# Kernel tuning notes

Measured on AMD Instinct MI355X. Metric: run time of the kernel, lower is better.

Reference implementation:

```python
import jax, jax.numpy as jnp
import numpy as np

B, L, H, NH = 2, 256, 1024, 16
HD = H // NH


def _ln(x, g, b, eps=1e-5):
    m = x.mean(-1, keepdims=True)
    v = x.var(-1, keepdims=True)
    return (x - m) * jax.lax.rsqrt(v + eps) * g + b


def setup_inputs() -> dict:
    key = jax.random.key(0)
    ks = jax.random.split(key, 24)
    s = 0.02
    inp = {
        'x': jax.random.normal(ks[0], (B, L, H), jnp.float32),
        'mask': jnp.ones((B, 1, 1, L), dtype=bool),
        'pos_emb': jax.random.normal(ks[1], (B, L, L, H), jnp.float32),
        'Wq': jax.random.normal(ks[2], (H, H), jnp.float32) * s,
        'bq': jnp.zeros((H,), jnp.float32),
        'Wk': jax.random.normal(ks[3], (H, H), jnp.float32) * s,
        'bk': jnp.zeros((H,), jnp.float32),
        'Wv': jax.random.normal(ks[4], (H, H), jnp.float32) * s,
        'bv': jnp.zeros((H,), jnp.float32),
        'Wr': jax.random.normal(ks[5], (H, H), jnp.float32) * s,
        'br': jnp.zeros((H,), jnp.float32),
        'u': jax.random.normal(ks[6], (NH, HD), jnp.float32) * s,
        'vb': jax.random.normal(ks[7], (NH, HD), jnp.float32) * s,
        'Wo': jax.random.normal(ks[8], (H, H), jnp.float32) * s,
        'bo': jnp.zeros((H,), jnp.float32),
        'ln1_g': jnp.ones((H,), jnp.float32),
        'ln1_b': jnp.zeros((H,), jnp.float32),
        'W1': jax.random.normal(ks[9], (3 * H, H), jnp.float32) * s,
        'b1': jnp.zeros((3 * H,), jnp.float32),
        'W2': jax.random.normal(ks[10], (H, 3 * H), jnp.float32) * s,
        'b2': jnp.zeros((H,), jnp.float32),
        'ln2_g': jnp.ones((H,), jnp.float32),
        'ln2_b': jnp.zeros((H,), jnp.float32),
    }
    return inp


def reference(x, mask, pos_emb, Wq, bq, Wk, bk, Wv, bv, Wr, br, u, vb, Wo, bo,
              ln1_g, ln1_b, W1, b1, W2, b2, ln2_g, ln2_b):
    b, l, h = x.shape
    nh, hd = NH, h // NH

    def heads(t):  # [B,L,H] -> [B,nh,L,hd]
        return t.reshape(b, l, nh, hd).transpose(0, 2, 1, 3)

    q = heads(x @ Wq.T + bq)
    k = heads(x @ Wk.T + bk)
    v = heads(x @ Wv.T + bv)
    # relative keys: [B,Lq,Lk,H] -> [B,Lq,Lk,nh,hd]
    rk = (pos_emb @ Wr.T + br).reshape(b, l, l, nh, hd)

    u4 = u[None, :, None, :]   # [1,nh,1,hd]
    v4 = vb[None, :, None, :]
    content = jnp.einsum('bhqd,bhkd->bhqk', q + u4, k)
    position = jnp.einsum('bhqd,bqkhd->bhqk', q + v4, rk)
    attn = jnp.where(mask, content + position, -1e6)
    attn = jax.nn.softmax(attn, axis=-1)  # attn_drop inactive (eval)

    out = jnp.einsum('bhqk,bhkd->bhqd', attn, v)
    out = out.transpose(0, 2, 1, 3).reshape(b, l, h)
    out = jax.nn.leaky_relu(out @ Wo.T + bo, 0.01) + x
    out = _ln(out, ln1_g, ln1_b)
    x2 = out
    out = jax.nn.leaky_relu(out @ W1.T + b1, 0.01) @ W2.T + b2
    out = _ln(out + x2, ln2_g, ln2_b)
    return out
```

## Files before the change

### kernel.cpp

```cpp
#include <hip/hip_runtime.h>
#include <cstdint>
#include <cstddef>

#define B_  2
#define L_  256
#define H_  1024
#define NH_ 16
#define HD_ 64
#define M_  (B_ * L_)

__device__ __forceinline__
void gemm64_body(const float* __restrict__ A, const float* __restrict__ Bw,
                 const float* __restrict__ bias, const float* __restrict__ resid,
                 float* __restrict__ C, int N, int K, int act,
                 int row0, int col0, float As[16][68], float Bs[16][68])
{
    const int tid = threadIdx.x;
    const int tx = tid & 15, ty = tid >> 4;
    const int lr = tid >> 2;
    const int lc = (tid & 3) * 4;
    float acc[4][4] = {};
    for (int k0 = 0; k0 < K; k0 += 16) {
        float4 av = *(const float4*)(A  + (size_t)(row0 + lr) * K + k0 + lc);
        float4 bv = *(const float4*)(Bw + (size_t)(col0 + lr) * K + k0 + lc);
        As[lc+0][lr] = av.x; As[lc+1][lr] = av.y; As[lc+2][lr] = av.z; As[lc+3][lr] = av.w;
        Bs[lc+0][lr] = bv.x; Bs[lc+1][lr] = bv.y; Bs[lc+2][lr] = bv.z; Bs[lc+3][lr] = bv.w;
        __syncthreads();
        #pragma unroll
        for (int kk = 0; kk < 16; ++kk) {
            float4 a4 = *(const float4*)&As[kk][ty * 4];
            float4 b4 = *(const float4*)&Bs[kk][tx * 4];
            float a[4] = {a4.x, a4.y, a4.z, a4.w};
            float b[4] = {b4.x, b4.y, b4.z, b4.w};
            #pragma unroll
            for (int i = 0; i < 4; ++i)
                #pragma unroll
                for (int j = 0; j < 4; ++j)
                    acc[i][j] = fmaf(a[i], b[j], acc[i][j]);
        }
        __syncthreads();
    }
    #pragma unroll
    for (int j = 0; j < 4; ++j) {
        const int c = col0 + tx * 4 + j;
        const float bj = bias ? bias[c] : 0.0f;
        #pragma unroll
        for (int i = 0; i < 4; ++i) {
            const int r = row0 + ty * 4 + i;
            float v = acc[i][j] + bj;
            if (act) v = v > 0.0f ? v : 0.01f * v;
            if (resid) v += resid[(size_t)r * N + c];
            C[(size_t)r * N + c] = v;
        }
    }
}

__global__ __launch_bounds__(256)
void gemm_bt(const float* __restrict__ A, const float* __restrict__ Bw,
             const float* __restrict__ bias, const float* __restrict__ resid,
             float* __restrict__ C, int M, int N, int K, int act)
{
    __shared__ float As[16][68];
    __shared__ float Bs[16][68];
    gemm64_body(A, Bw, bias, resid, C, N, K, act,
                blockIdx.y * 64, blockIdx.x * 64, As, Bs);
}

__global__ __launch_bounds__(256)
void qkv_kernel(const float* __restrict__ x,
                const float* __restrict__ Wq, const float* __restrict__ bq,
                const float* __restrict__ Wk, const float* __restrict__ bk,
                const float* __restrict__ Wv, const float* __restrict__ bv,
                float* __restrict__ qb, float* __restrict__ kb, float* __restrict__ vbuf)
{
    __shared__ float As[16][68];
    __shared__ float Bs[16][68];
    const int z = blockIdx.z;
    const float* Bw   = (z == 0) ? Wq : (z == 1) ? Wk : Wv;
    const float* bias = (z == 0) ? bq : (z == 1) ? bk : bv;
    float*       C    = (z == 0) ? qb : (z == 1) ? kb : vbuf;
    gemm64_body(x, Bw, bias, nullptr, C, H_, H_, 0,
                blockIdx.y * 64, blockIdx.x * 64, As, Bs);
}

__global__ __launch_bounds__(256)
void s_kernel(const float* __restrict__ qbuf, const float* __restrict__ vb,
              const float* __restrict__ Wr, float* __restrict__ sbuf)
{
    __shared__ float As[64][68];
    __shared__ float Bs[64][68];
    const int tid = threadIdx.x;
    const int h  = blockIdx.z;
    const int e0 = blockIdx.x * 64;
    const int m0 = blockIdx.y * 64;
    #pragma unroll
    for (int p = 0; p < 4; ++p) {
        int f4 = tid + p * 256;
        int r  = f4 >> 4;
        int c  = (f4 & 15) * 4;
        float4 qv  = *(const float4*)(qbuf + (size_t)(m0 + r) * H_ + h * HD_ + c);
        float4 vbv = *(const float4*)(vb + h * HD_ + c);
        As[c+0][r] = qv.x + vbv.x; As[c+1][r] = qv.y + vbv.y;
        As[c+2][r] = qv.z + vbv.z; As[c+3][r] = qv.w + vbv.w;
        float4 wv = *(const float4*)(Wr + (size_t)(h * HD_ + r) * H_ + e0 + c);
        *(float4*)&Bs[r][c] = wv;
    }
    __syncthreads();
    const int tx = tid & 15, ty = tid >> 4;
    float acc[4][4] = {};
    #pragma unroll 16
    for (int kk = 0; kk < 64; ++kk) {
        float4 a4 = *(const float4*)&As[kk][ty * 4];
        float4 b4 = *(const float4*)&Bs[kk][tx * 4];
        float a[4] = {a4.x, a4.y, a4.z, a4.w};
        float b[4] = {b4.x, b4.y, b4.z, b4.w};
        #pragma unroll
        for (int i = 0; i < 4; ++i)
            #pragma unroll
            for (int j = 0; j < 4; ++j)
                acc[i][j] = fmaf(a[i], b[j], acc[i][j]);
    }
    #pragma unroll
    for (int i = 0; i < 4; ++i)
        #pragma unroll
        for (int j = 0; j < 4; ++j)
            sbuf[((size_t)(m0 + ty*4 + i) * NH_ + h) * H_ + e0 + tx*4 + j] = acc[i][j];
}

__global__ __launch_bounds__(256)
void cpos_kernel(const float* __restrict__ qbuf, const float* __restrict__ vb,
                 const float* __restrict__ br, float* __restrict__ cpos)
{
    const int idx = blockIdx.x * 256 + threadIdx.x;
    const int m = idx >> 4, h = idx & 15;
    float s = 0.0f;
    #pragma unroll 8
    for (int d = 0; d < HD_; ++d)
        s += (qbuf[(size_t)m * H_ + h * HD_ + d] + vb[h * HD_ + d]) * br[h * HD_ + d];
    cpos[idx] = s;
}

__global__ __launch_bounds__(256)
void content_kernel(const float* __restrict__ qbuf, const float* __restrict__ kbuf,
                    const float* __restrict__ u, const float* __restrict__ cpos,
                    float* __restrict__ scores)
{
    __shared__ float As[64][68];
    __shared__ float Bs[64][68];
    const int tid = threadIdx.x;
    const int bh = blockIdx.z; const int b = bh >> 4, h = bh & 15;
    const int q0 = blockIdx.y * 64, k0 = blockIdx.x * 64;
    #pragma unroll
    for (int p = 0; p < 4; ++p) {
        int f4 = tid + p * 256;
        int r  = f4 >> 4;
        int c  = (f4 & 15) * 4;
        float4 qv = *(const float4*)(qbuf + (size_t)(b * L_ + q0 + r) * H_ + h * HD_ + c);
        float4 uv = *(const float4*)(u + h * HD_ + c);
        As[c+0][r] = qv.x + uv.x; As[c+1][r] = qv.y + uv.y;
        As[c+2][r] = qv.z + uv.z; As[c+3][r] = qv.w + uv.w;
        float4 kv = *(const float4*)(kbuf + (size_t)(b * L_ + k0 + r) * H_ + h * HD_ + c);
        Bs[c+0][r] = kv.x; Bs[c+1][r] = kv.y; Bs[c+2][r] = kv.z; Bs[c+3][r] = kv.w;
    }
    __syncthreads();
    const int tx = tid & 15, ty = tid >> 4;
    float acc[4][4] = {};
    #pragma unroll 16
    for (int kk = 0; kk < 64; ++kk) {
        float4 a4 = *(const float4*)&As[kk][ty * 4];
        float4 b4 = *(const float4*)&Bs[kk][tx * 4];
        float a[4] = {a4.x, a4.y, a4.z, a4.w};
        float b[4] = {b4.x, b4.y, b4.z, b4.w};
        #pragma unroll
        for (int i = 0; i < 4; ++i)
            #pragma unroll
            for (int j = 0; j < 4; ++j)
                acc[i][j] = fmaf(a[i], b[j], acc[i][j]);
    }
    #pragma unroll
    for (int i = 0; i < 4; ++i) {
        const int qrow = q0 + ty * 4 + i;
        const float cp = cpos[(size_t)(b * L_ + qrow) * NH_ + h];
        #pragma unroll
        for (int j = 0; j < 4; ++j)
            scores[(((size_t)b * NH_ + h) * L_ + qrow) * L_ + k0 + tx*4 + j] = acc[i][j] + cp;
    }
}

__global__ __launch_bounds__(256)
void pos_kernel(const float* __restrict__ sbuf, const float* __restrict__ pos_emb,
                float* __restrict__ scores)
{
    __shared__ float sP[128][33];
    __shared__ float sS[16][33];
    const int m = blockIdx.x;
    const int b = m >> 8, q = m & 255;
    const int kb0 = blockIdx.y * 128;
    const int tid = threadIdx.x;
    const int hg = tid >> 6;
    const int kg = tid & 63;
    float acc[4][2] = {};
    for (int e0 = 0; e0 < H_; e0 += 32) {
        {
            int hh = tid >> 4;
            int e2 = (tid & 15) * 2;
            float2 sv = *(const float2*)(sbuf + ((size_t)m * NH_ + hh) * H_ + e0 + e2);
            sS[hh][e2] = sv.x; sS[hh][e2 + 1] = sv.y;
        }
        #pragma unroll
        for (int p = 0; p < 4; ++p) {
            int idx = p * 256 + tid;
            int row = idx >> 3;
            int e4  = (idx & 7) * 4;
            float4 pv = *(const float4*)(pos_emb + ((size_t)m * L_ + kb0 + row) * H_ + e0 + e4);
            sP[row][e4+0] = pv.x; sP[row][e4+1] = pv.y; sP[row][e4+2] = pv.z; sP[row][e4+3] = pv.w;
        }
        __syncthreads();
        #pragma unroll
        for (int e = 0; e < 32; ++e) {
            float sv[4], pv[2];
            #pragma unroll
            for (int j = 0; j < 4; ++j) sv[j] = sS[hg * 4 + j][e];
            #pragma unroll
            for (int i = 0; i < 2; ++i) pv[i] = sP[kg + i * 64][e];
            #pragma unroll
            for (int j = 0; j < 4; ++j)
                #pragma unroll
                for (int i = 0; i < 2; ++i)
                    acc[j][i] = fmaf(sv[j], pv[i], acc[j][i]);
        }
        __syncthreads();
    }
    #pragma unroll
    for (int j = 0; j < 4; ++j) {
        const int h = hg * 4 + j;
        #pragma unroll
        for (int i = 0; i < 2; ++i) {
            const int k = kb0 + kg + i * 64;
            scores[(((size_t)b * NH_ + h) * L_ + q) * L_ + k] += acc[j][i];
        }
    }
}

__global__ __launch_bounds__(64)
void softmax_kernel(float* __restrict__ scores)
{
    const size_t row = blockIdx.x;
    const int t = threadIdx.x;
    float4 v = *(float4*)(scores + row * L_ + t * 4);
    float mx = fmaxf(fmaxf(v.x, v.y), fmaxf(v.z, v.w));
    #pragma unroll
    for (int off = 32; off >= 1; off >>= 1) mx = fmaxf(mx, __shfl_xor(mx, off));
    v.x = __expf(v.x - mx); v.y = __expf(v.y - mx);
    v.z = __expf(v.z - mx); v.w = __expf(v.w - mx);
    float s = v.x + v.y + v.z + v.w;
    #pragma unroll
    for (int off = 32; off >= 1; off >>= 1) s += __shfl_xor(s, off);
    const float inv = 1.0f / s;
    v.x *= inv; v.y *= inv; v.z *= inv; v.w *= inv;
    *(float4*)(scores + row * L_ + t * 4) = v;
}

__global__ __launch_bounds__(256)
void attnv_kernel(const float* __restrict__ scores, const float* __restrict__ vbuf,
                  float* __restrict__ attno)
{
    __shared__ float As[64][68];
    __shared__ float Bs[64][68];
    const int bh = blockIdx.y; const int b = bh >> 4, h = bh & 15;
    const int q0 = blockIdx.x * 64;
    const int tid = threadIdx.x;
    const int tx = tid & 15, ty = tid >> 4;
    float acc[4][4] = {};
    for (int k0 = 0; k0 < L_; k0 += 64) {
        #pragma unroll
        for (int p = 0; p < 4; ++p) {
            int f4 = tid + p * 256;
            int r  = f4 >> 4;
            int c  = (f4 & 15) * 4;
            float4 pv = *(const float4*)(scores + (((size_t)b * NH_ + h) * L_ + q0 + r) * L_ + k0 + c);
            As[c+0][r] = pv.x; As[c+1][r] = pv.y; As[c+2][r] = pv.z; As[c+3][r] = pv.w;
            float4 vv = *(const float4*)(vbuf + (size_t)(b * L_ + k0 + r) * H_ + h * HD_ + c);
            *(float4*)&Bs[r][c] = vv;
        }
        __syncthreads();
        #pragma unroll 16
        for (int kk = 0; kk < 64; ++kk) {
            float4 a4 = *(const float4*)&As[kk][ty * 4];
            float4 b4 = *(const float4*)&Bs[kk][tx * 4];
            float a[4] = {a4.x, a4.y, a4.z, a4.w};
            float bb[4] = {b4.x, b4.y, b4.z, b4.w};
            #pragma unroll
            for (int i = 0; i < 4; ++i)
                #pragma unroll
                for (int j = 0; j < 4; ++j)
                    acc[i][j] = fmaf(a[i], bb[j], acc[i][j]);
        }
        __syncthreads();
    }
    #pragma unroll
    for (int i = 0; i < 4; ++i)
        #pragma unroll
        for (int j = 0; j < 4; ++j)
            attno[(size_t)(b * L_ + q0 + ty*4 + i) * H_ + h * HD_ + tx*4 + j] = acc[i][j];
}

__global__ __launch_bounds__(256)
void ln_kernel(const float* __restrict__ in, const float* __restrict__ resid,
               const float* __restrict__ g, const float* __restrict__ bias,
               float* __restrict__ out)
{
    __shared__ float rsum[4], rsum2[4];
    const size_t row = blockIdx.x;
    const int tid = threadIdx.x;
    float4 v = *(const float4*)(in + row * H_ + tid * 4);
    if (resid) {
        float4 r = *(const float4*)(resid + row * H_ + tid * 4);
        v.x += r.x; v.y += r.y; v.z += r.z; v.w += r.w;
    }
    float s  = v.x + v.y + v.z + v.w;
    float s2 = v.x*v.x + v.y*v.y + v.z*v.z + v.w*v.w;
    #pragma unroll
    for (int off = 32; off >= 1; off >>= 1) {
        s  += __shfl_xor(s, off);
        s2 += __shfl_xor(s2, off);
    }
    const int w = tid >> 6;
    if ((tid & 63) == 0) { rsum[w] = s; rsum2[w] = s2; }
    __syncthreads();
    s  = rsum[0] + rsum[1] + rsum[2] + rsum[3];
    s2 = rsum2[0] + rsum2[1] + rsum2[2] + rsum2[3];
    const float mean = s * (1.0f / H_);
    const float var  = s2 * (1.0f / H_) - mean * mean;
    const float rs   = rsqrtf(var + 1e-5f);
    float4 gv = *(const float4*)(g + tid * 4);
    float4 bv = *(const float4*)(bias + tid * 4);
    float4 o;
    o.x = (v.x - mean) * rs * gv.x + bv.x;
    o.y = (v.y - mean) * rs * gv.y + bv.y;
    o.z = (v.z - mean) * rs * gv.z + bv.z;
    o.w = (v.w - mean) * rs * gv.w + bv.w;
    *(float4*)(out + row * H_ + tid * 4) = o;
}

extern "C" void kernel_launch(void* const* d_in, const int* in_sizes, int n_in,
                              void* d_out, int out_size, void* d_ws, size_t ws_size,
                              hipStream_t stream)
{
    const float* x       = (const float*)d_in[0];
    const float* pos_emb = (const float*)d_in[2];
    const float* Wq = (const float*)d_in[3];  const float* bq = (const float*)d_in[4];
    const float* Wk = (const float*)d_in[5];  const float* bk = (const float*)d_in[6];
    const float* Wv = (const float*)d_in[7];  const float* bv = (const float*)d_in[8];
    const float* Wr = (const float*)d_in[9];  const float* br = (const float*)d_in[10];
    const float* u  = (const float*)d_in[11]; const float* vb = (const float*)d_in[12];
    const float* Wo = (const float*)d_in[13]; const float* bo = (const float*)d_in[14];
    const float* g1 = (const float*)d_in[15]; const float* be1 = (const float*)d_in[16];
    const float* W1 = (const float*)d_in[17]; const float* b1 = (const float*)d_in[18];
    const float* W2 = (const float*)d_in[19]; const float* b2 = (const float*)d_in[20];
    const float* g2 = (const float*)d_in[21]; const float* be2 = (const float*)d_in[22];
    float* outp = (float*)d_out;

    float* ws     = (float*)d_ws;
    float* qbuf   = ws;
    float* kbuf   = qbuf + (size_t)M_ * H_;
    float* vbuf   = kbuf + (size_t)M_ * H_;
    float* sbuf   = vbuf + (size_t)M_ * H_;
    float* cpos   = sbuf + (size_t)M_ * NH_ * H_;
    float* scores = cpos + (size_t)M_ * NH_;
    float* attno  = scores + (size_t)B_ * NH_ * L_ * L_;
    float* o1     = attno + (size_t)M_ * H_;
    float* x2     = o1 + (size_t)M_ * H_;
    float* hid    = x2 + (size_t)M_ * H_;
    float* o2     = hid + (size_t)M_ * 3 * H_;

    dim3 thr(256);

    qkv_kernel<<<dim3(16, 8, 3), thr, 0, stream>>>(x, Wq, bq, Wk, bk, Wv, bv,
                                                   qbuf, kbuf, vbuf);

    s_kernel<<<dim3(16, 8, 16), thr, 0, stream>>>(qbuf, vb, Wr, sbuf);
    cpos_kernel<<<dim3(32), thr, 0, stream>>>(qbuf, vb, br, cpos);

    content_kernel<<<dim3(4, 4, 32), thr, 0, stream>>>(qbuf, kbuf, u, cpos, scores);
    pos_kernel<<<dim3(M_, 2), thr, 0, stream>>>(sbuf, pos_emb, scores);

    softmax_kernel<<<dim3(B_ * NH_ * L_), dim3(64), 0, stream>>>(scores);
    attnv_kernel<<<dim3(4, 32), thr, 0, stream>>>(scores, vbuf, attno);

    gemm_bt<<<dim3(16, 8), thr, 0, stream>>>(attno, Wo, bo, x, o1, M_, H_, H_, 1);
    ln_kernel<<<dim3(M_), thr, 0, stream>>>(o1, nullptr, g1, be1, x2);

    gemm_bt<<<dim3(48, 8), thr, 0, stream>>>(x2, W1, b1, nullptr, hid, M_, 3 * H_, H_, 1);
    gemm_bt<<<dim3(16, 8), thr, 0, stream>>>(hid, W2, b2, nullptr, o2, M_, H_, 3 * H_, 0);
    ln_kernel<<<dim3(M_), thr, 0, stream>>>(o2, x2, g2, be2, outp);
}
```

Baseline: 1.231 ms.

## Replace LDS-tiled GEMMs with direct-load dot4 kernels, split-K, and restructured pos kernel

The shared-memory tiled GEMMs are replaced by register-only kernels that read float4 strips of A and W straight from global memory, relying on cache for reuse. The Wo and W2 projections use a two-way split-K, and their partial sums are reduced inside fused layernorm kernels that also apply bias, activation and residual. The pos-score kernel now splits the embedding dimension in half, keeps all 16 heads in registers per thread, and writes two partial score planes. The softmax sums those planes, which replaces the read-modify-write on scores. In exchange it uses more workspace and extra partial-buffer traffic, and the direct global loads may cost more than the old LDS tiling.

```diff
diff --git a/kernel.cpp b/kernel.cpp
--- a/kernel.cpp
+++ b/kernel.cpp
@@ -10,77 +10,139 @@
 #define M_  (B_ * L_)
 
 __device__ __forceinline__
-void gemm64_body(const float* __restrict__ A, const float* __restrict__ Bw,
-                 const float* __restrict__ bias, const float* __restrict__ resid,
-                 float* __restrict__ C, int N, int K, int act,
-                 int row0, int col0, float As[16][68], float Bs[16][68])
-{
-    const int tid = threadIdx.x;
-    const int tx = tid & 15, ty = tid >> 4;
-    const int lr = tid >> 2;
-    const int lc = (tid & 3) * 4;
-    float acc[4][4] = {};
-    for (int k0 = 0; k0 < K; k0 += 16) {
-        float4 av = *(const float4*)(A  + (size_t)(row0 + lr) * K + k0 + lc);
-        float4 bv = *(const float4*)(Bw + (size_t)(col0 + lr) * K + k0 + lc);
-        As[lc+0][lr] = av.x; As[lc+1][lr] = av.y; As[lc+2][lr] = av.z; As[lc+3][lr] = av.w;
-        Bs[lc+0][lr] = bv.x; Bs[lc+1][lr] = bv.y; Bs[lc+2][lr] = bv.z; Bs[lc+3][lr] = bv.w;
-        __syncthreads();
-        #pragma unroll
-        for (int kk = 0; kk < 16; ++kk) {
-            float4 a4 = *(const float4*)&As[kk][ty * 4];
-            float4 b4 = *(const float4*)&Bs[kk][tx * 4];
-            float a[4] = {a4.x, a4.y, a4.z, a4.w};
-            float b[4] = {b4.x, b4.y, b4.z, b4.w};
-            #pragma unroll
-            for (int i = 0; i < 4; ++i)
-                #pragma unroll
-                for (int j = 0; j < 4; ++j)
-                    acc[i][j] = fmaf(a[i], b[j], acc[i][j]);
-        }
-        __syncthreads();
-    }
+void dot4_core(const float* __restrict__ A, int lda,
+               const float* __restrict__ Bw, int ldb,
+               int kBeg, int kEnd, int row0, int col0,
+               float acc[4][4])
+{
+    const int tx = threadIdx.x & 15, ty = threadIdx.x >> 4;
+    const float* a0 = A + (size_t)(row0 + ty * 4) * lda;
+    const float* b0 = Bw + (size_t)(col0 + tx * 4) * ldb;
+    #pragma unroll 4
+    for (int k0 = kBeg; k0 < kEnd; k0 += 4) {
+        float4 a[4], b[4];
+        #pragma unroll
+        for (int i = 0; i < 4; ++i) a[i] = *(const float4*)(a0 + (size_t)i * lda + k0);
+        #pragma unroll
+        for (int j = 0; j < 4; ++j) b[j] = *(const float4*)(b0 + (size_t)j * ldb + k0);
+        #pragma unroll
+        for (int i = 0; i < 4; ++i)
+            #pragma unroll
+            for (int j = 0; j < 4; ++j) {
+                acc[i][j] = fmaf(a[i].x, b[j].x, acc[i][j]);
+                acc[i][j] = fmaf(a[i].y, b[j].y, acc[i][j]);
+                acc[i][j] = fmaf(a[i].z, b[j].z, acc[i][j]);
+                acc[i][j] = fmaf(a[i].w, b[j].w, acc[i][j]);
+            }
+    }
+}
+
+__global__ __launch_bounds__(256)
+void qkv_dot4(const float* __restrict__ x,
+              const float* __restrict__ Wq, const float* __restrict__ bq,
+              const float* __restrict__ Wk, const float* __restrict__ bk,
+              const float* __restrict__ Wv, const float* __restrict__ bv,
+              float* __restrict__ qb, float* __restrict__ kb, float* __restrict__ vb)
+{
+    const int z = blockIdx.z;
+    const float* W    = (z == 0) ? Wq : (z == 1) ? Wk : Wv;
+    const float* bias = (z == 0) ? bq : (z == 1) ? bk : bv;
+    float*       C    = (z == 0) ? qb : (z == 1) ? kb : vb;
+    const int row0 = blockIdx.y * 64, col0 = blockIdx.x * 64;
+    float acc[4][4] = {};
+    dot4_core(x, H_, W, H_, 0, H_, row0, col0, acc);
+    const int tx = threadIdx.x & 15, ty = threadIdx.x >> 4;
     #pragma unroll
     for (int j = 0; j < 4; ++j) {
         const int c = col0 + tx * 4 + j;
-        const float bj = bias ? bias[c] : 0.0f;
+        const float bj = bias[c];
+        #pragma unroll
+        for (int i = 0; i < 4; ++i)
+            C[(size_t)(row0 + ty * 4 + i) * H_ + c] = acc[i][j] + bj;
+    }
+}
+
+__global__ __launch_bounds__(256)
+void w1_dot4(const float* __restrict__ x2, const float* __restrict__ W1,
+             const float* __restrict__ b1, float* __restrict__ hid)
+{
+    const int row0 = blockIdx.y * 64, col0 = blockIdx.x * 64;
+    float acc[4][4] = {};
+    dot4_core(x2, H_, W1, H_, 0, H_, row0, col0, acc);
+    const int tx = threadIdx.x & 15, ty = threadIdx.x >> 4;
+    #pragma unroll
+    for (int j = 0; j < 4; ++j) {
+        const int c = col0 + tx * 4 + j;
+        const float bj = b1[c];
         #pragma unroll
         for (int i = 0; i < 4; ++i) {
-            const int r = row0 + ty * 4 + i;
             float v = acc[i][j] + bj;
-            if (act) v = v > 0.0f ? v : 0.01f * v;
-            if (resid) v += resid[(size_t)r * N + c];
-            C[(size_t)r * N + c] = v;
-        }
-    }
-}
-
-__global__ __launch_bounds__(256)
-void gemm_bt(const float* __restrict__ A, const float* __restrict__ Bw,
-             const float* __restrict__ bias, const float* __restrict__ resid,
-             float* __restrict__ C, int M, int N, int K, int act)
-{
-    __shared__ float As[16][68];
-    __shared__ float Bs[16][68];
-    gemm64_body(A, Bw, bias, resid, C, N, K, act,
-                blockIdx.y * 64, blockIdx.x * 64, As, Bs);
-}
-
-__global__ __launch_bounds__(256)
-void qkv_kernel(const float* __restrict__ x,
-                const float* __restrict__ Wq, const float* __restrict__ bq,
-                const float* __restrict__ Wk, const float* __restrict__ bk,
-                const float* __restrict__ Wv, const float* __restrict__ bv,
-                float* __restrict__ qb, float* __restrict__ kb, float* __restrict__ vbuf)
-{
-    __shared__ float As[16][68];
-    __shared__ float Bs[16][68];
+            v = v > 0.0f ? v : 0.01f * v;
+            hid[(size_t)(row0 + ty * 4 + i) * (3 * H_) + c] = v;
+        }
+    }
+}
+
+__global__ __launch_bounds__(256)
+void gemm_dot4_splitk(const float* __restrict__ A, int K,
+                      const float* __restrict__ W, int N,
+                      float* __restrict__ pbase)
+{
     const int z = blockIdx.z;
-    const float* Bw   = (z == 0) ? Wq : (z == 1) ? Wk : Wv;
-    const float* bias = (z == 0) ? bq : (z == 1) ? bk : bv;
-    float*       C    = (z == 0) ? qb : (z == 1) ? kb : vbuf;
-    gemm64_body(x, Bw, bias, nullptr, C, H_, H_, 0,
-                blockIdx.y * 64, blockIdx.x * 64, As, Bs);
+    const int kh = K >> 1;
+    const int row0 = blockIdx.y * 64, col0 = blockIdx.x * 64;
+    float acc[4][4] = {};
+    dot4_core(A, K, W, K, z * kh, z * kh + kh, row0, col0, acc);
+    float* C = pbase + (size_t)z * M_ * N;
+    const int tx = threadIdx.x & 15, ty = threadIdx.x >> 4;
+    #pragma unroll
+    for (int j = 0; j < 4; ++j)
+        #pragma unroll
+        for (int i = 0; i < 4; ++i)
+            C[(size_t)(row0 + ty * 4 + i) * N + col0 + tx * 4 + j] = acc[i][j];
+}
+
+__global__ __launch_bounds__(256)
+void content_dot4(const float* __restrict__ qbuf, const float* __restrict__ kbuf,
+                  const float* __restrict__ u, const float* __restrict__ cpos,
+                  float* __restrict__ scores)
+{
+    const int bh = blockIdx.z; const int b = bh >> 4, h = bh & 15;
+    const int q0 = blockIdx.y * 64, k0 = blockIdx.x * 64;
+    const int tx = threadIdx.x & 15, ty = threadIdx.x >> 4;
+    const float* A  = qbuf + (size_t)(b * L_ + q0 + ty * 4) * H_ + h * HD_;
+    const float* Bp = kbuf + (size_t)(b * L_ + k0 + tx * 4) * H_ + h * HD_;
+    const float* up = u + h * HD_;
+    float acc[4][4] = {};
+    #pragma unroll 4
+    for (int d0 = 0; d0 < HD_; d0 += 4) {
+        float4 uu = *(const float4*)(up + d0);
+        float4 a[4], bb[4];
+        #pragma unroll
+        for (int i = 0; i < 4; ++i) {
+            a[i] = *(const float4*)(A + (size_t)i * H_ + d0);
+            a[i].x += uu.x; a[i].y += uu.y; a[i].z += uu.z; a[i].w += uu.w;
+        }
+        #pragma unroll
+        for (int j = 0; j < 4; ++j) bb[j] = *(const float4*)(Bp + (size_t)j * H_ + d0);
+        #pragma unroll
+        for (int i = 0; i < 4; ++i)
+            #pragma unroll
+            for (int j = 0; j < 4; ++j) {
+                acc[i][j] = fmaf(a[i].x, bb[j].x, acc[i][j]);
+                acc[i][j] = fmaf(a[i].y, bb[j].y, acc[i][j]);
+                acc[i][j] = fmaf(a[i].z, bb[j].z, acc[i][j]);
+                acc[i][j] = fmaf(a[i].w, bb[j].w, acc[i][j]);
+            }
+    }
+    #pragma unroll
+    for (int i = 0; i < 4; ++i) {
+        const int qrow = q0 + ty * 4 + i;
+        const float cp = cpos[(size_t)(b * L_ + qrow) * NH_ + h];
+        #pragma unroll
+        for (int j = 0; j < 4; ++j)
+            scores[(((size_t)b * NH_ + h) * L_ + qrow) * L_ + k0 + tx * 4 + j] = acc[i][j] + cp;
+    }
 }
 
 __global__ __launch_bounds__(256)
@@ -141,124 +203,117 @@
 }
 
 __global__ __launch_bounds__(256)
-void content_kernel(const float* __restrict__ qbuf, const float* __restrict__ kbuf,
-                    const float* __restrict__ u, const float* __restrict__ cpos,
-                    float* __restrict__ scores)
-{
-    __shared__ float As[64][68];
-    __shared__ float Bs[64][68];
+void pos_v2(const float* __restrict__ sbuf, const float* __restrict__ pos_emb,
+            float* __restrict__ pp)
+{
+    __shared__ float sP[256][33];
+    __shared__ float sS[32][16];
+    const int m = blockIdx.x;  const int b = m >> 8, q = m & 255;
+    const int eh = blockIdx.y;
     const int tid = threadIdx.x;
-    const int bh = blockIdx.z; const int b = bh >> 4, h = bh & 15;
-    const int q0 = blockIdx.y * 64, k0 = blockIdx.x * 64;
-    #pragma unroll
-    for (int p = 0; p < 4; ++p) {
-        int f4 = tid + p * 256;
-        int r  = f4 >> 4;
-        int c  = (f4 & 15) * 4;
-        float4 qv = *(const float4*)(qbuf + (size_t)(b * L_ + q0 + r) * H_ + h * HD_ + c);
-        float4 uv = *(const float4*)(u + h * HD_ + c);
-        As[c+0][r] = qv.x + uv.x; As[c+1][r] = qv.y + uv.y;
-        As[c+2][r] = qv.z + uv.z; As[c+3][r] = qv.w + uv.w;
-        float4 kv = *(const float4*)(kbuf + (size_t)(b * L_ + k0 + r) * H_ + h * HD_ + c);
-        Bs[c+0][r] = kv.x; Bs[c+1][r] = kv.y; Bs[c+2][r] = kv.z; Bs[c+3][r] = kv.w;
+    const int w = tid >> 6, lane = tid & 63;
+    const float* Pm = pos_emb + (size_t)m * L_ * H_;
+    const float* Sm = sbuf + (size_t)m * NH_ * H_;
+    float acc[16][4] = {};
+    for (int c = 0; c < 16; ++c) {
+        const int e0 = eh * 512 + c * 32;
+        if (tid < 128) {
+            int hh = tid >> 3;
+            int e4 = (tid & 7) * 4;
+            float4 sv = *(const float4*)(Sm + (size_t)hh * H_ + e0 + e4);
+            sS[e4+0][hh] = sv.x; sS[e4+1][hh] = sv.y;
+            sS[e4+2][hh] = sv.z; sS[e4+3][hh] = sv.w;
+        }
+        #pragma unroll
+        for (int p = 0; p < 8; ++p) {
+            int idx = p * 256 + tid;
+            int kk = idx >> 3;
+            int ec = (idx & 7) * 4;
+            float4 pv = *(const float4*)(Pm + (size_t)kk * H_ + e0 + ec);
+            sP[kk][ec+0] = pv.x; sP[kk][ec+1] = pv.y;
+            sP[kk][ec+2] = pv.z; sP[kk][ec+3] = pv.w;
+        }
+        __syncthreads();
+        #pragma unroll
+        for (int ee = 0; ee < 8; ++ee) {
+            const int el = w * 8 + ee;
+            float s[16];
+            #pragma unroll
+            for (int j4 = 0; j4 < 4; ++j4) {
+                float4 s4 = *(const float4*)&sS[el][j4 * 4];
+                s[j4*4+0] = s4.x; s[j4*4+1] = s4.y; s[j4*4+2] = s4.z; s[j4*4+3] = s4.w;
+            }
+            #pragma unroll
+            for (int i = 0; i < 4; ++i) {
+                const float pk = sP[lane + i * 64][el];
+                #pragma unroll
+                for (int h = 0; h < 16; ++h)
+                    acc[h][i] = fmaf(s[h], pk, acc[h][i]);
+            }
+        }
+        __syncthreads();
+    }
+    float* red = &sP[0][0];
+    if (w >= 2) {
+        float* dst = red + (size_t)(w - 2) * 4096;
+        #pragma unroll
+        for (int h = 0; h < 16; ++h)
+            #pragma unroll
+            for (int i = 0; i < 4; ++i)
+                dst[(h * 4 + i) * 64 + lane] = acc[h][i];
     }
     __syncthreads();
-    const int tx = tid & 15, ty = tid >> 4;
-    float acc[4][4] = {};
-    #pragma unroll 16
-    for (int kk = 0; kk < 64; ++kk) {
-        float4 a4 = *(const float4*)&As[kk][ty * 4];
-        float4 b4 = *(const float4*)&Bs[kk][tx * 4];
-        float a[4] = {a4.x, a4.y, a4.z, a4.w};
-        float b[4] = {b4.x, b4.y, b4.z, b4.w};
-        #pragma unroll
-        for (int i = 0; i < 4; ++i)
-            #pragma unroll
-            for (int j = 0; j < 4; ++j)
-                acc[i][j] = fmaf(a[i], b[j], acc[i][j]);
-    }
-    #pragma unroll
-    for (int i = 0; i < 4; ++i) {
-        const int qrow = q0 + ty * 4 + i;
-        const float cp = cpos[(size_t)(b * L_ + qrow) * NH_ + h];
-        #pragma unroll
-        for (int j = 0; j < 4; ++j)
-            scores[(((size_t)b * NH_ + h) * L_ + qrow) * L_ + k0 + tx*4 + j] = acc[i][j] + cp;
-    }
-}
-
-__global__ __launch_bounds__(256)
-void pos_kernel(const float* __restrict__ sbuf, const float* __restrict__ pos_emb,
-                float* __restrict__ scores)
-{
-    __shared__ float sP[128][33];
-    __shared__ float sS[16][33];
-    const int m = blockIdx.x;
-    const int b = m >> 8, q = m & 255;
-    const int kb0 = blockIdx.y * 128;
-    const int tid = threadIdx.x;
-    const int hg = tid >> 6;
-    const int kg = tid & 63;
-    float acc[4][2] = {};
-    for (int e0 = 0; e0 < H_; e0 += 32) {
-        {
-            int hh = tid >> 4;
-            int e2 = (tid & 15) * 2;
-            float2 sv = *(const float2*)(sbuf + ((size_t)m * NH_ + hh) * H_ + e0 + e2);
-            sS[hh][e2] = sv.x; sS[hh][e2 + 1] = sv.y;
-        }
-        #pragma unroll
-        for (int p = 0; p < 4; ++p) {
-            int idx = p * 256 + tid;
-            int row = idx >> 3;
-            int e4  = (idx & 7) * 4;
-            float4 pv = *(const float4*)(pos_emb + ((size_t)m * L_ + kb0 + row) * H_ + e0 + e4);
-            sP[row][e4+0] = pv.x; sP[row][e4+1] = pv.y; sP[row][e4+2] = pv.z; sP[row][e4+3] = pv.w;
-        }
-        __syncthreads();
-        #pragma unroll
-        for (int e = 0; e < 32; ++e) {
-            float sv[4], pv[2];
-            #pragma unroll
-            for (int j = 0; j < 4; ++j) sv[j] = sS[hg * 4 + j][e];
-            #pragma unroll
-            for (int i = 0; i < 2; ++i) pv[i] = sP[kg + i * 64][e];
-            #pragma unroll
-            for (int j = 0; j < 4; ++j)
-                #pragma unroll
-                for (int i = 0; i < 2; ++i)
-                    acc[j][i] = fmaf(sv[j], pv[i], acc[j][i]);
-        }
-        __syncthreads();
-    }
-    #pragma unroll
-    for (int j = 0; j < 4; ++j) {
-        const int h = hg * 4 + j;
-        #pragma unroll
-        for (int i = 0; i < 2; ++i) {
-            const int k = kb0 + kg + i * 64;
-            scores[(((size_t)b * NH_ + h) * L_ + q) * L_ + k] += acc[j][i];
-        }
+    if (w < 2) {
+        const float* src = red + (size_t)w * 4096;
+        #pragma unroll
+        for (int h = 0; h < 16; ++h)
+            #pragma unroll
+            for (int i = 0; i < 4; ++i)
+                acc[h][i] += src[(h * 4 + i) * 64 + lane];
+    }
+    __syncthreads();
+    if (w == 1) {
+        #pragma unroll
+        for (int h = 0; h < 16; ++h)
+            #pragma unroll
+            for (int i = 0; i < 4; ++i)
+                red[(h * 4 + i) * 64 + lane] = acc[h][i];
+    }
+    __syncthreads();
+    if (w == 0) {
+        float* ppe = pp + (size_t)eh * B_ * NH_ * L_ * L_;
+        #pragma unroll
+        for (int h = 0; h < 16; ++h)
+            #pragma unroll
+            for (int i = 0; i < 4; ++i) {
+                float vsum = acc[h][i] + red[(h * 4 + i) * 64 + lane];
+                ppe[(((size_t)(b * NH_ + h)) * L_ + q) * L_ + lane + i * 64] = vsum;
+            }
     }
 }
 
 __global__ __launch_bounds__(64)
-void softmax_kernel(float* __restrict__ scores)
+void softmax3(float* __restrict__ scores, const float* __restrict__ pp0,
+              const float* __restrict__ pp1)
 {
     const size_t row = blockIdx.x;
     const int t = threadIdx.x;
-    float4 v = *(float4*)(scores + row * L_ + t * 4);
+    const size_t off = row * L_ + t * 4;
+    float4 v = *(float4*)(scores + off);
+    float4 a = *(const float4*)(pp0 + off);
+    float4 b = *(const float4*)(pp1 + off);
+    v.x += a.x + b.x; v.y += a.y + b.y; v.z += a.z + b.z; v.w += a.w + b.w;
     float mx = fmaxf(fmaxf(v.x, v.y), fmaxf(v.z, v.w));
     #pragma unroll
-    for (int off = 32; off >= 1; off >>= 1) mx = fmaxf(mx, __shfl_xor(mx, off));
+    for (int off2 = 32; off2 >= 1; off2 >>= 1) mx = fmaxf(mx, __shfl_xor(mx, off2));
     v.x = __expf(v.x - mx); v.y = __expf(v.y - mx);
     v.z = __expf(v.z - mx); v.w = __expf(v.w - mx);
     float s = v.x + v.y + v.z + v.w;
     #pragma unroll
-    for (int off = 32; off >= 1; off >>= 1) s += __shfl_xor(s, off);
+    for (int off2 = 32; off2 >= 1; off2 >>= 1) s += __shfl_xor(s, off2);
     const float inv = 1.0f / s;
     v.x *= inv; v.y *= inv; v.z *= inv; v.w *= inv;
-    *(float4*)(scores + row * L_ + t * 4) = v;
+    *(float4*)(scores + off) = v;
 }
 
 __global__ __launch_bounds__(256)
@@ -305,19 +360,11 @@
             attno[(size_t)(b * L_ + q0 + ty*4 + i) * H_ + h * HD_ + tx*4 + j] = acc[i][j];
 }
 
-__global__ __launch_bounds__(256)
-void ln_kernel(const float* __restrict__ in, const float* __restrict__ resid,
-               const float* __restrict__ g, const float* __restrict__ bias,
-               float* __restrict__ out)
+__device__ __forceinline__
+void ln_core(float4 v, const float* __restrict__ g, const float* __restrict__ bias,
+             float* __restrict__ out, size_t row, int tid)
 {
     __shared__ float rsum[4], rsum2[4];
-    const size_t row = blockIdx.x;
-    const int tid = threadIdx.x;
-    float4 v = *(const float4*)(in + row * H_ + tid * 4);
-    if (resid) {
-        float4 r = *(const float4*)(resid + row * H_ + tid * 4);
-        v.x += r.x; v.y += r.y; v.z += r.z; v.w += r.w;
-    }
     float s  = v.x + v.y + v.z + v.w;
     float s2 = v.x*v.x + v.y*v.y + v.z*v.z + v.w*v.w;
     #pragma unroll
@@ -343,6 +390,48 @@
     *(float4*)(out + row * H_ + tid * 4) = o;
 }
 
+__global__ __launch_bounds__(256)
+void ln1_fuse(const float* __restrict__ p0, const float* __restrict__ p1,
+              const float* __restrict__ bo, const float* __restrict__ x,
+              const float* __restrict__ g, const float* __restrict__ bias,
+              float* __restrict__ out)
+{
+    const size_t row = blockIdx.x;
+    const int tid = threadIdx.x;
+    const size_t off = row * H_ + tid * 4;
+    float4 a = *(const float4*)(p0 + off);
+    float4 b = *(const float4*)(p1 + off);
+    float4 bb = *(const float4*)(bo + tid * 4);
+    float4 xx = *(const float4*)(x + off);
+    float4 v;
+    v.x = a.x + b.x + bb.x; v.y = a.y + b.y + bb.y;
+    v.z = a.z + b.z + bb.z; v.w = a.w + b.w + bb.w;
+    v.x = (v.x > 0.f ? v.x : 0.01f * v.x) + xx.x;
+    v.y = (v.y > 0.f ? v.y : 0.01f * v.y) + xx.y;
+    v.z = (v.z > 0.f ? v.z : 0.01f * v.z) + xx.z;
+    v.w = (v.w > 0.f ? v.w : 0.01f * v.w) + xx.w;
+    ln_core(v, g, bias, out, row, tid);
+}
+
+__global__ __launch_bounds__(256)
+void ln2_fuse(const float* __restrict__ p0, const float* __restrict__ p1,
+              const float* __restrict__ b2, const float* __restrict__ x2,
+              const float* __restrict__ g, const float* __restrict__ bias,
+              float* __restrict__ out)
+{
+    const size_t row = blockIdx.x;
+    const int tid = threadIdx.x;
+    const size_t off = row * H_ + tid * 4;
+    float4 a = *(const float4*)(p0 + off);
+    float4 b = *(const float4*)(p1 + off);
+    float4 bb = *(const float4*)(b2 + tid * 4);
+    float4 xx = *(const float4*)(x2 + off);
+    float4 v;
+    v.x = a.x + b.x + bb.x + xx.x; v.y = a.y + b.y + bb.y + xx.y;
+    v.z = a.z + b.z + bb.z + xx.z; v.w = a.w + b.w + bb.w + xx.w;
+    ln_core(v, g, bias, out, row, tid);
+}
+
 extern "C" void kernel_launch(void* const* d_in, const int* in_sizes, int n_in,
                               void* d_out, int out_size, void* d_ws, size_t ws_size,
                               hipStream_t stream)
@@ -363,35 +452,36 @@
 
     float* ws     = (float*)d_ws;
     float* qbuf   = ws;
-    float* kbuf   = qbuf + (size_t)M_ * H_;
-    float* vbuf   = kbuf + (size_t)M_ * H_;
-    float* sbuf   = vbuf + (size_t)M_ * H_;
-    float* cpos   = sbuf + (size_t)M_ * NH_ * H_;
-    float* scores = cpos + (size_t)M_ * NH_;
-    float* attno  = scores + (size_t)B_ * NH_ * L_ * L_;
-    float* o1     = attno + (size_t)M_ * H_;
-    float* x2     = o1 + (size_t)M_ * H_;
-    float* hid    = x2 + (size_t)M_ * H_;
-    float* o2     = hid + (size_t)M_ * 3 * H_;
+    float* kbuf   = qbuf  + (size_t)M_ * H_;
+    float* vbuf   = kbuf  + (size_t)M_ * H_;
+    float* sbuf   = vbuf  + (size_t)M_ * H_;
+    float* cpos   = sbuf  + (size_t)M_ * NH_ * H_;
+    float* scores = cpos  + (size_t)M_ * NH_;
+    float* pp     = scores + (size_t)B_ * NH_ * L_ * L_;
+    float* attno  = pp    + (size_t)2 * B_ * NH_ * L_ * L_;
+    float* o1p    = attno + (size_t)M_ * H_;
+    float* x2     = o1p   + (size_t)2 * M_ * H_;
+    float* hid    = x2    + (size_t)M_ * H_;
+    float* o2p    = hid   + (size_t)M_ * 3 * H_;
 
     dim3 thr(256);
 
-    qkv_kernel<<<dim3(16, 8, 3), thr, 0, stream>>>(x, Wq, bq, Wk, bk, Wv, bv,
-                                                   qbuf, kbuf, vbuf);
-
+    qkv_dot4<<<dim3(16, 8, 3), thr, 0, stream>>>(x, Wq, bq, Wk, bk, Wv, bv,
+                                                 qbuf, kbuf, vbuf);
     s_kernel<<<dim3(16, 8, 16), thr, 0, stream>>>(qbuf, vb, Wr, sbuf);
     cpos_kernel<<<dim3(32), thr, 0, stream>>>(qbuf, vb, br, cpos);
 
-    content_kernel<<<dim3(4, 4, 32), thr, 0, stream>>>(qbuf, kbuf, u, cpos, scores);
-    pos_kernel<<<dim3(M_, 2), thr, 0, stream>>>(sbuf, pos_emb, scores);
-
-    softmax_kernel<<<dim3(B_ * NH_ * L_), dim3(64), 0, stream>>>(scores);
+    content_dot4<<<dim3(4, 4, 32), thr, 0, stream>>>(qbuf, kbuf, u, cpos, scores);
+    pos_v2<<<dim3(M_, 2), thr, 0, stream>>>(sbuf, pos_emb, pp);
+
+    softmax3<<<dim3(B_ * NH_ * L_), dim3(64), 0, stream>>>(
+        scores, pp, pp + (size_t)B_ * NH_ * L_ * L_);
     attnv_kernel<<<dim3(4, 32), thr, 0, stream>>>(scores, vbuf, attno);
 
-    gemm_bt<<<dim3(16, 8), thr, 0, stream>>>(attno, Wo, bo, x, o1, M_, H_, H_, 1);
-    ln_kernel<<<dim3(M_), thr, 0, stream>>>(o1, nullptr, g1, be1, x2);
-
-    gemm_bt<<<dim3(48, 8), thr, 0, stream>>>(x2, W1, b1, nullptr, hid, M_, 3 * H_, H_, 1);
-    gemm_bt<<<dim3(16, 8), thr, 0, stream>>>(hid, W2, b2, nullptr, o2, M_, H_, 3 * H_, 0);
-    ln_kernel<<<dim3(M_), thr, 0, stream>>>(o2, x2, g2, be2, outp);
-}
+    gemm_dot4_splitk<<<dim3(16, 8, 2), thr, 0, stream>>>(attno, H_, Wo, H_, o1p);
+    ln1_fuse<<<dim3(M_), thr, 0, stream>>>(o1p, o1p + (size_t)M_ * H_, bo, x, g1, be1, x2);
+
+    w1_dot4<<<dim3(48, 8), thr, 0, stream>>>(x2, W1, b1, hid);
+    gemm_dot4_splitk<<<dim3(16, 8, 2), thr, 0, stream>>>(hid, 3 * H_, W2, H_, o2p);
+    ln2_fuse<<<dim3(M_), thr, 0, stream>>>(o2p, o2p + (size_t)M_ * H_, b2, x2, g2, be2, outp);
+}
```

Result: slower. 1.813 ms (+47.3%).
